# Optimization experiments

Measured on AMD Instinct MI355X. Metric: run time of the kernel, lower is better.

Reference implementation:

```python
import jax, jax.numpy as jnp
import numpy as np

N_CLASSES = 2
N_FEATURES = 100
PSI_DIM = 10
BATCH = 500000


def setup_inputs() -> dict:
    key = jax.random.key(0)
    k_x, k_ar, k_ai, k_pr, k_pi = jax.random.split(key, 5)
    x = jax.random.normal(k_x, (BATCH, N_FEATURES), dtype=jnp.float32)
    A_real = jax.random.normal(k_ar, (N_CLASSES, PSI_DIM, PSI_DIM, N_FEATURES), dtype=jnp.float32)
    A_imag = jax.random.normal(k_ai, (N_CLASSES, PSI_DIM, PSI_DIM, N_FEATURES), dtype=jnp.float32)
    psi_real = jax.random.normal(k_pr, (PSI_DIM,), dtype=jnp.float32)
    psi_imag = jax.random.normal(k_pi, (PSI_DIM,), dtype=jnp.float32)
    return {"x": x, "A_real": A_real, "A_imag": A_imag, "psi_real": psi_real, "psi_imag": psi_imag}


def reference(x, A_real, A_imag, psi_real, psi_imag):
    # result_{tk} = Re[ sum_{i,j,a} conj(psi)_i A_{kija} x_{ta} psi_j ]  (x is real)
    # P_{ij} = conj(psi)_i psi_j ; expand in real arithmetic to avoid complex tensors.
    P_re = jnp.outer(psi_real, psi_real) + jnp.outer(psi_imag, psi_imag)   # [i,j]
    P_im = jnp.outer(psi_real, psi_imag) - jnp.outer(psi_imag, psi_real)   # [i,j]
    # Re(M)_{ka} = sum_{ij} P_re A_real - P_im A_imag  -> tiny [2,100] matrix
    M_re = jnp.einsum('ij,kija->ka', P_re, A_real) - jnp.einsum('ij,kija->ka', P_im, A_imag)
    # out_{tk} = sum_a x_{ta} Re(M)_{ka} : memory-bound [t,100] x [100,2]
    return jnp.einsum('ta,ka->tk', x, M_re)
```

## Files before the change

kernel.cpp:

```cpp
#include <hip/hip_runtime.h>

#define NF      100
#define BLOCK   128
#define TILE    64
#define F4T     (TILE * 25)
#define NLD     13
#define F4PAD   (NLD * BLOCK)
#define NBUF    3
#define MAXGRID 512

__device__ __forceinline__ void stage_tile(const float4* __restrict__ x4,
                                           float4* dst, int f4base, int maxf4,
                                           int tid) {
#pragma unroll
  for (int u = 0; u < NLD; ++u) {
    int g = f4base + u * BLOCK + tid;
    g = g > maxf4 ? maxf4 : g;
    __builtin_amdgcn_global_load_lds(
        (const __attribute__((address_space(1))) void*)(x4 + g),
        (__attribute__((address_space(3))) void*)(dst + u * BLOCK + tid),
        16, 0, 0);
  }
}

#define WAITCNT_VM14_LGKM0 0x007E

__global__ __launch_bounds__(BLOCK, 1) void fused_kernel(
    const float4* __restrict__ x4,
    const float* __restrict__ A_real, const float* __restrict__ A_imag,
    const float* __restrict__ psi_real, const float* __restrict__ psi_imag,
    float2* __restrict__ out, int batch, int ntiles) {
  __shared__ float4 xs[NBUF][F4PAD];
  __shared__ __align__(16) float2 msl[NF];

  const int tid = threadIdx.x;
  const int maxf4 = batch * 25 - 1;
  const int stride = gridDim.x;

  float4* b0 = &xs[0][0];
  float4* b1 = &xs[1][0];
  float4* b2 = &xs[2][0];

  int t = blockIdx.x;
  stage_tile(x4, b0, t * F4T, maxf4, tid);
  stage_tile(x4, b1, (t + stride) * F4T, maxf4, tid);

  if (tid < NF) {
    const int a = tid;
    float pr[10], pi[10];
#pragma unroll
    for (int i = 0; i < 10; ++i) { pr[i] = psi_real[i]; pi[i] = psi_imag[i]; }
    float m0 = 0.f, m1 = 0.f;
#pragma unroll
    for (int i = 0; i < 10; ++i) {
#pragma unroll
      for (int j = 0; j < 10; ++j) {
        float pre = pr[i] * pr[j] + pi[i] * pi[j];
        float pim = pr[i] * pi[j] - pi[i] * pr[j];
        int off = (i * 10 + j) * NF + a;
        m0 = fmaf(pre, A_real[off], m0);
        m0 = fmaf(-pim, A_imag[off], m0);
        m1 = fmaf(pre, A_real[off + 10000], m1);
        m1 = fmaf(-pim, A_imag[off + 10000], m1);
      }
    }
    msl[a] = make_float2(m0, m1);
  }
  __syncthreads();

  const int h = tid & 1;
  const int r = tid >> 1;
  const float4* msl4 = (const float4*)msl;
  float4 mreg[26];
#pragma unroll
  for (int j = 0; j < 26; ++j) mreg[j] = msl4[24 * h + j];

  for (; t < ntiles; t += stride) {
    __builtin_amdgcn_s_waitcnt(WAITCNT_VM14_LGKM0);
    __builtin_amdgcn_s_barrier();

    stage_tile(x4, b2, (t + 2 * stride) * F4T, maxf4, tid);

    const float4* xrow = b0 + r * 25 + (h ? 12 : 0);
    float a0 = 0.f, a1 = 0.f;
#pragma unroll
    for (int j = 0; j < 13; ++j) {
      if (j < 12 + h) {
        float4 xv = xrow[j];
        float4 mA = mreg[2 * j];
        float4 mB = mreg[2 * j + 1];
        a0 = fmaf(xv.x, mA.x, a0); a1 = fmaf(xv.x, mA.y, a1);
        a0 = fmaf(xv.y, mA.z, a0); a1 = fmaf(xv.y, mA.w, a1);
        a0 = fmaf(xv.z, mB.x, a0); a1 = fmaf(xv.z, mB.y, a1);
        a0 = fmaf(xv.w, mB.z, a0); a1 = fmaf(xv.w, mB.w, a1);
      }
    }
    a0 += __shfl_xor(a0, 1);
    a1 += __shfl_xor(a1, 1);
    const int t0 = t * TILE;
    if (h == 0 && r < batch - t0) out[t0 + r] = make_float2(a0, a1);

    float4* tmp = b0; b0 = b1; b1 = b2; b2 = tmp;
  }
}

extern "C" void kernel_launch(void* const* d_in, const int* in_sizes, int n_in,
                              void* d_out, int out_size, void* d_ws, size_t ws_size,
                              hipStream_t stream) {
  const float* x  = (const float*)d_in[0];
  const float* Ar = (const float*)d_in[1];
  const float* Ai = (const float*)d_in[2];
  const float* pr = (const float*)d_in[3];
  const float* pi = (const float*)d_in[4];
  const int batch = in_sizes[0] / NF;

  const int ntiles = (batch + TILE - 1) / TILE;
  const int grid = ntiles < MAXGRID ? ntiles : MAXGRID;
  fused_kernel<<<grid, BLOCK, 0, stream>>>(
      (const float4*)x, Ar, Ai, pr, pi, (float2*)d_out, batch, ntiles);
}
```

Measured before the change: 285.7 us.

## Use single-wave blocks with one thread per row and no shuffle reduction

```diff
diff --git a/kernel.cpp b/kernel.cpp
--- a/kernel.cpp
+++ b/kernel.cpp
@@ -1,11 +1,10 @@
 #include <hip/hip_runtime.h>
 
 #define NF      100
-#define BLOCK   128
+#define BLOCK   64
 #define TILE    64
 #define F4T     (TILE * 25)
-#define NLD     13
-#define F4PAD   (NLD * BLOCK)
+#define NLD     25
 #define NBUF    3
 #define MAXGRID 512
 
@@ -23,14 +22,14 @@
   }
 }
 
-#define WAITCNT_VM14_LGKM0 0x007E
+#define WAITCNT_VM26 0x4F7A
 
 __global__ __launch_bounds__(BLOCK, 1) void fused_kernel(
     const float4* __restrict__ x4,
     const float* __restrict__ A_real, const float* __restrict__ A_imag,
     const float* __restrict__ psi_real, const float* __restrict__ psi_imag,
     float2* __restrict__ out, int batch, int ntiles) {
-  __shared__ float4 xs[NBUF][F4PAD];
+  __shared__ float4 xs[NBUF][F4T];
   __shared__ __align__(16) float2 msl[NF];
 
   const int tid = threadIdx.x;
@@ -45,60 +44,61 @@
   stage_tile(x4, b0, t * F4T, maxf4, tid);
   stage_tile(x4, b1, (t + stride) * F4T, maxf4, tid);
 
-  if (tid < NF) {
-    const int a = tid;
+  {
     float pr[10], pi[10];
 #pragma unroll
     for (int i = 0; i < 10; ++i) { pr[i] = psi_real[i]; pi[i] = psi_imag[i]; }
-    float m0 = 0.f, m1 = 0.f;
+    const bool two = tid < (NF - BLOCK);
+    float m0 = 0.f, m1 = 0.f, n0 = 0.f, n1 = 0.f;
 #pragma unroll
     for (int i = 0; i < 10; ++i) {
 #pragma unroll
       for (int j = 0; j < 10; ++j) {
         float pre = pr[i] * pr[j] + pi[i] * pi[j];
         float pim = pr[i] * pi[j] - pi[i] * pr[j];
-        int off = (i * 10 + j) * NF + a;
+        int off = (i * 10 + j) * NF + tid;
         m0 = fmaf(pre, A_real[off], m0);
         m0 = fmaf(-pim, A_imag[off], m0);
         m1 = fmaf(pre, A_real[off + 10000], m1);
         m1 = fmaf(-pim, A_imag[off + 10000], m1);
+        if (two) {
+          n0 = fmaf(pre, A_real[off + BLOCK], n0);
+          n0 = fmaf(-pim, A_imag[off + BLOCK], n0);
+          n1 = fmaf(pre, A_real[off + BLOCK + 10000], n1);
+          n1 = fmaf(-pim, A_imag[off + BLOCK + 10000], n1);
+        }
       }
     }
-    msl[a] = make_float2(m0, m1);
+    msl[tid] = make_float2(m0, m1);
+    if (two) msl[tid + BLOCK] = make_float2(n0, n1);
   }
   __syncthreads();
 
-  const int h = tid & 1;
-  const int r = tid >> 1;
   const float4* msl4 = (const float4*)msl;
-  float4 mreg[26];
+  float4 mreg[50];
 #pragma unroll
-  for (int j = 0; j < 26; ++j) mreg[j] = msl4[24 * h + j];
+  for (int j = 0; j < 50; ++j) mreg[j] = msl4[j];
 
   for (; t < ntiles; t += stride) {
-    __builtin_amdgcn_s_waitcnt(WAITCNT_VM14_LGKM0);
+    __builtin_amdgcn_s_waitcnt(WAITCNT_VM26);
     __builtin_amdgcn_s_barrier();
 
     stage_tile(x4, b2, (t + 2 * stride) * F4T, maxf4, tid);
 
-    const float4* xrow = b0 + r * 25 + (h ? 12 : 0);
+    const float4* xrow = b0 + tid * 25;
     float a0 = 0.f, a1 = 0.f;
 #pragma unroll
-    for (int j = 0; j < 13; ++j) {
-      if (j < 12 + h) {
-        float4 xv = xrow[j];
-        float4 mA = mreg[2 * j];
-        float4 mB = mreg[2 * j + 1];
-        a0 = fmaf(xv.x, mA.x, a0); a1 = fmaf(xv.x, mA.y, a1);
-        a0 = fmaf(xv.y, mA.z, a0); a1 = fmaf(xv.y, mA.w, a1);
-        a0 = fmaf(xv.z, mB.x, a0); a1 = fmaf(xv.z, mB.y, a1);
-        a0 = fmaf(xv.w, mB.z, a0); a1 = fmaf(xv.w, mB.w, a1);
-      }
+    for (int j = 0; j < 25; ++j) {
+      float4 xv = xrow[j];
+      float4 mA = mreg[2 * j];
+      float4 mB = mreg[2 * j + 1];
+      a0 = fmaf(xv.x, mA.x, a0); a1 = fmaf(xv.x, mA.y, a1);
+      a0 = fmaf(xv.y, mA.z, a0); a1 = fmaf(xv.y, mA.w, a1);
+      a0 = fmaf(xv.z, mB.x, a0); a1 = fmaf(xv.z, mB.y, a1);
+      a0 = fmaf(xv.w, mB.z, a0); a1 = fmaf(xv.w, mB.w, a1);
     }
-    a0 += __shfl_xor(a0, 1);
-    a1 += __shfl_xor(a1, 1);
     const int t0 = t * TILE;
-    if (h == 0 && r < batch - t0) out[t0 + r] = make_float2(a0, a1);
+    if (tid < batch - t0) out[t0 + tid] = make_float2(a0, a1);
 
     float4* tmp = b0; b0 = b1; b1 = b2; b2 = tmp;
   }
```

Result: slower. 393.0 us (+37.6%).

## Halve tile to 32 rows, split each row across 4 lanes, raise grid

Applied to the files above, without the earlier changes.

```diff
diff --git a/kernel.cpp b/kernel.cpp
--- a/kernel.cpp
+++ b/kernel.cpp
@@ -2,28 +2,29 @@
 
 #define NF      100
 #define BLOCK   128
-#define TILE    64
+#define TILE    32
 #define F4T     (TILE * 25)
-#define NLD     13
+#define NLD     7
 #define F4PAD   (NLD * BLOCK)
 #define NBUF    3
-#define MAXGRID 512
+#define MAXGRID 768
 
 __device__ __forceinline__ void stage_tile(const float4* __restrict__ x4,
                                            float4* dst, int f4base, int maxf4,
                                            int tid) {
 #pragma unroll
   for (int u = 0; u < NLD; ++u) {
-    int g = f4base + u * BLOCK + tid;
+    int idx = u * BLOCK + tid;
+    int g = f4base + (idx < F4T ? idx : 0);
     g = g > maxf4 ? maxf4 : g;
     __builtin_amdgcn_global_load_lds(
         (const __attribute__((address_space(1))) void*)(x4 + g),
-        (__attribute__((address_space(3))) void*)(dst + u * BLOCK + tid),
+        (__attribute__((address_space(3))) void*)(dst + idx),
         16, 0, 0);
   }
 }
 
-#define WAITCNT_VM14_LGKM0 0x007E
+#define WAITCNT_VM8_NOLGKM 0x0F78
 
 __global__ __launch_bounds__(BLOCK, 1) void fused_kernel(
     const float4* __restrict__ x4,
@@ -68,37 +69,42 @@
   }
   __syncthreads();
 
-  const int h = tid & 1;
-  const int r = tid >> 1;
+  const int q = tid & 3;
+  const int r = tid >> 2;
   const float4* msl4 = (const float4*)msl;
-  float4 mreg[26];
+  float4 mreg[14];
 #pragma unroll
-  for (int j = 0; j < 26; ++j) mreg[j] = msl4[24 * h + j];
+  for (int i = 0; i < 7; ++i) {
+    int j = q + 4 * i;
+    int jc = j < 25 ? j : 24;
+    mreg[2 * i]     = msl4[2 * jc];
+    mreg[2 * i + 1] = msl4[2 * jc + 1];
+  }
 
   for (; t < ntiles; t += stride) {
-    __builtin_amdgcn_s_waitcnt(WAITCNT_VM14_LGKM0);
+    __builtin_amdgcn_s_waitcnt(WAITCNT_VM8_NOLGKM);
     __builtin_amdgcn_s_barrier();
 
     stage_tile(x4, b2, (t + 2 * stride) * F4T, maxf4, tid);
 
-    const float4* xrow = b0 + r * 25 + (h ? 12 : 0);
+    const float4* xrow = b0 + r * 25 + q;
     float a0 = 0.f, a1 = 0.f;
 #pragma unroll
-    for (int j = 0; j < 13; ++j) {
-      if (j < 12 + h) {
-        float4 xv = xrow[j];
-        float4 mA = mreg[2 * j];
-        float4 mB = mreg[2 * j + 1];
+    for (int i = 0; i < 7; ++i) {
+      if (i < 6 || q == 0) {
+        float4 xv = xrow[4 * i];
+        float4 mA = mreg[2 * i];
+        float4 mB = mreg[2 * i + 1];
         a0 = fmaf(xv.x, mA.x, a0); a1 = fmaf(xv.x, mA.y, a1);
         a0 = fmaf(xv.y, mA.z, a0); a1 = fmaf(xv.y, mA.w, a1);
         a0 = fmaf(xv.z, mB.x, a0); a1 = fmaf(xv.z, mB.y, a1);
         a0 = fmaf(xv.w, mB.z, a0); a1 = fmaf(xv.w, mB.w, a1);
       }
     }
-    a0 += __shfl_xor(a0, 1);
-    a1 += __shfl_xor(a1, 1);
+    a0 += __shfl_xor(a0, 1); a0 += __shfl_xor(a0, 2);
+    a1 += __shfl_xor(a1, 1); a1 += __shfl_xor(a1, 2);
     const int t0 = t * TILE;
-    if (h == 0 && r < batch - t0) out[t0 + r] = make_float2(a0, a1);
+    if (q == 0 && r < batch - t0) out[t0 + r] = make_float2(a0, a1);
 
     float4* tmp = b0; b0 = b1; b1 = b2; b2 = tmp;
   }
```

Measured after the change: 288.0 us. No clear change (+0.8%).
